# Optimization experiments

Measured on AMD Instinct MI355X. Metric: run time of the kernel, lower is better.

## Reference

```python
import jax, jax.numpy as jnp
import numpy as np

DIM = 2048
NH = 16
NKV = 4
HD = DIM // NH            # 128
KVD = HD * NKV            # 512
MLP = int(DIM * 4.0 * 2 / 3)  # 5461
EPS = 1.1920929e-07       # torch.finfo(float32).eps (nn.RMSNorm default)
ROPE_BASE = 10000.0


def act_quant(x):
    # per-token int8 absmax quantization (BitNet b1.58)
    scale = 127.0 / jnp.clip(jnp.max(jnp.abs(x), axis=-1, keepdims=True), 1e-5)
    return jnp.clip(jnp.round(x * scale), -128.0, 127.0) / scale


def weight_quant(w):
    # ternary weights via mean-absmax scale (BitNet b1.58)
    scale = 1.0 / jnp.clip(jnp.mean(jnp.abs(w)), 1e-5)
    return jnp.clip(jnp.round(w * scale), -1.0, 1.0) / scale


def bitlinear(x, w, b=None):
    # straight-through estimator quantization, then dense matmul
    xq = x + jax.lax.stop_gradient(act_quant(x) - x)
    wq = w + jax.lax.stop_gradient(weight_quant(w) - w)
    y = xq @ wq.T
    return y if b is None else y + b


def rmsnorm(x, w):
    return x * jax.lax.rsqrt(jnp.mean(x * x, axis=-1, keepdims=True) + EPS) * w


def rope_cos_sin(pos, head_dim, dtype):
    inv_freq = 1.0 / (ROPE_BASE ** (jnp.arange(0, head_dim, 2, dtype=jnp.float32) / head_dim))
    freqs = pos[..., None].astype(jnp.float32) * inv_freq  # [B,N,HD/2]
    cos = jnp.repeat(jnp.cos(freqs), 2, axis=-1).astype(dtype)  # interleaved [B,N,HD]
    sin = jnp.repeat(jnp.sin(freqs), 2, axis=-1).astype(dtype)
    return cos, sin


def rotate_interleave(x):
    x1 = x[..., 0::2]
    x2 = x[..., 1::2]
    return jnp.stack([-x2, x1], axis=-1).reshape(x.shape)


def apply_rope(x, cos, sin):
    # x: [B,H,N,HD]; cos/sin: [B,N,HD]
    return x * cos[:, None] + rotate_interleave(x) * sin[:, None]


def setup_inputs() -> dict:
    key = jax.random.key(0)
    ks = jax.random.split(key, 16)
    B, N = 2, 2048
    s = 0.02
    return {
        "x": jax.random.normal(ks[0], (B, N, DIM), jnp.float32),
        "position_ids": jnp.broadcast_to(jnp.arange(N, dtype=jnp.int32), (B, N)),
        "norm1_w": jnp.ones((DIM,), jnp.float32),
        "q_w": jax.random.normal(ks[1], (DIM, DIM), jnp.float32) * s,
        "q_b": jnp.zeros((DIM,), jnp.float32),
        "k_w": jax.random.normal(ks[2], (KVD, DIM), jnp.float32) * s,
        "k_b": jnp.zeros((KVD,), jnp.float32),
        "v_w": jax.random.normal(ks[3], (KVD, DIM), jnp.float32) * s,
        "v_b": jnp.zeros((KVD,), jnp.float32),
        "o_w": jax.random.normal(ks[4], (DIM, DIM), jnp.float32) * s,
        "norm2_w": jnp.ones((DIM,), jnp.float32),
        "gate_w": jax.random.normal(ks[5], (MLP, DIM), jnp.float32) * s,
        "up_w": jax.random.normal(ks[6], (MLP, DIM), jnp.float32) * s,
        "down_w": jax.random.normal(ks[7], (DIM, MLP), jnp.float32) * s,
    }


def reference(x, position_ids, norm1_w, q_w, q_b, k_w, k_b, v_w, v_b, o_w,
              norm2_w, gate_w, up_w, down_w):
    B, N, C = x.shape
    # --- attention ---
    h = rmsnorm(x, norm1_w)
    q = bitlinear(h, q_w, q_b).reshape(B, N, NH, HD).transpose(0, 2, 1, 3)
    k = bitlinear(h, k_w, k_b).reshape(B, N, NKV, HD).transpose(0, 2, 1, 3)
    v = bitlinear(h, v_w, v_b).reshape(B, N, NKV, HD).transpose(0, 2, 1, 3)
    cos, sin = rope_cos_sin(position_ids, HD, x.dtype)
    q = apply_rope(q, cos, sin)
    k = apply_rope(k, cos, sin)
    g = NH // NKV
    k = jnp.repeat(k, g, axis=1)  # GQA head expansion -> [B,NH,N,HD]
    v = jnp.repeat(v, g, axis=1)
    scores = jnp.einsum('bhqd,bhkd->bhqk', q, k) * (HD ** -0.5)
    causal_mask = jnp.triu(jnp.ones((N, N), bool), 1)
    scores = jnp.where(causal_mask, -jnp.inf, scores)
    attn = jax.nn.softmax(scores, axis=-1)
    out = jnp.einsum('bhqk,bhkd->bqhd', attn, v).reshape(B, N, C)
    x = x + bitlinear(out, o_w)
    # --- SwiGLU MLP ---
    h = rmsnorm(x, norm2_w)
    x = x + bitlinear(jax.nn.silu(bitlinear(h, gate_w)) * bitlinear(h, up_w), down_w)
    return x
```

## Files before the change

kernel.cpp:

```cpp
#include <hip/hip_runtime.h>

typedef unsigned short u16;
typedef unsigned int   u32;
typedef unsigned char  u8;

using bf16x8 = __attribute__((ext_vector_type(8))) short;
using f32x4  = __attribute__((ext_vector_type(4))) float;
using i32x4  = __attribute__((ext_vector_type(4))) int;

#define SEQ    2048
#define DIMC   2048
#define TOK    4096
#define QKV_N  3072
#define GU_N   11008
#define MLP_P  5504
#define MLP_R  5461
#define ATT_SCALE 0.08838834764831845f

__device__ __forceinline__ float bf2f(u16 v){ return __uint_as_float(((u32)v) << 16); }
__device__ __forceinline__ u16 f2bf(float f){
  u32 x = __float_as_uint(f);
  u32 r = (x + 0x7fffu + ((x >> 16) & 1u)) >> 16;
  return (u16)r;
}

__device__ __forceinline__ float waveRedSum(float v){
#pragma unroll
  for (int o = 32; o > 0; o >>= 1) v += __shfl_xor(v, o);
  return v;
}
__device__ __forceinline__ float waveRedMax(float v){
#pragma unroll
  for (int o = 32; o > 0; o >>= 1) v = fmaxf(v, __shfl_xor(v, o));
  return v;
}

#define GLD16(gp, lp) __builtin_amdgcn_global_load_lds( \
    (__attribute__((address_space(1))) void*)(gp), \
    (__attribute__((address_space(3))) void*)(lp), 16, 0, 0)

#define FENCE() asm volatile("" ::: "memory")
#define SBAR()  do{ FENCE(); __builtin_amdgcn_s_barrier(); FENCE(); }while(0)
#define VMCNT(n) asm volatile("s_waitcnt vmcnt(" #n ")" ::: "memory")

__global__ __launch_bounds__(256) void k_abssum7(
    const float4* __restrict__ w0, const float4* __restrict__ w1,
    const float4* __restrict__ w2, const float4* __restrict__ w3,
    const float4* __restrict__ w4, const float4* __restrict__ w5,
    const float4* __restrict__ w6, float* __restrict__ sc){
  const int rg = blockIdx.y;
  const float4* w = rg==0?w0: rg==1?w1: rg==2?w2: rg==3?w3: rg==4?w4: rg==5?w5: w6;
  const int n4 = (rg==0||rg==3) ? 1048576 : (rg<4 ? 262144 : 2796032);
  float s = 0.f;
  for (int i = blockIdx.x*256 + threadIdx.x; i < n4; i += gridDim.x*256){
    float4 v = w[i];
    s += fabsf(v.x) + fabsf(v.y) + fabsf(v.z) + fabsf(v.w);
  }
  s = waveRedSum(s);
  __shared__ float sm[4];
  int lane = threadIdx.x & 63, wv = threadIdx.x >> 6;
  if (lane == 0) sm[wv] = s;
  __syncthreads();
  if (threadIdx.x == 0) atomicAdd(sc + rg, sm[0]+sm[1]+sm[2]+sm[3]);
}

__global__ void k_finalize(float* __restrict__ sc){
  if (threadIdx.x == 0){
    const float counts[7] = {4194304.f, 1048576.f, 1048576.f, 4194304.f,
                             11184128.f, 11184128.f, 11184128.f};
    for (int i = 0; i < 7; i++) sc[8+i] = fmaxf(sc[i]/counts[i], 1e-5f);
  }
}

__global__ __launch_bounds__(256) void k_wquant6(
    const float4* __restrict__ w0, const float4* __restrict__ w1,
    const float4* __restrict__ w2, const float4* __restrict__ w3,
    const float4* __restrict__ w4, const float4* __restrict__ w5,
    u32* __restrict__ d0, u32* __restrict__ d1, u32* __restrict__ d2,
    u32* __restrict__ d3, u32* __restrict__ dgu,
    const float* __restrict__ sc){
  const int rg = blockIdx.y;
  const float4* src = rg==0?w0: rg==1?w1: rg==2?w2: rg==3?w3: rg==4?w4: w5;
  const int n4 = (rg==0||rg==3) ? 1048576 : (rg<4 ? 262144 : 2796032);
  float ws = 1.0f / sc[8+rg];
  for (int i = blockIdx.x*256 + threadIdx.x; i < n4; i += gridDim.x*256){
    float4 v = src[i];
    int c0 = (int)fminf(fmaxf(rintf(v.x*ws), -1.f), 1.f);
    int c1 = (int)fminf(fmaxf(rintf(v.y*ws), -1.f), 1.f);
    int c2 = (int)fminf(fmaxf(rintf(v.z*ws), -1.f), 1.f);
    int c3 = (int)fminf(fmaxf(rintf(v.w*ws), -1.f), 1.f);
    u32 pk = (u32)(u8)c0 | ((u32)(u8)c1 << 8) | ((u32)(u8)c2 << 16) | ((u32)(u8)c3 << 24);
    if (rg < 4){
      u32* dst = rg==0?d0: rg==1?d1: rg==2?d2: d3;
      dst[i] = pk;
    } else {
      int row = i >> 9, col = i & 511;
      int rI = 32*(row>>4) + (row&15) + ((rg==5)?16:0);
      dgu[(long)rI*512 + col] = pk;
    }
  }
}

__global__ __launch_bounds__(256) void k_wquant_down(const float* __restrict__ src,
                                                     u32* __restrict__ dst,
                                                     const float* __restrict__ deqp){
  int i = blockIdx.x*256 + threadIdx.x;
  const int total = 2048*(MLP_P/4);
  if (i >= total) return;
  float ws = 1.0f / deqp[0];
  int r = i / (MLP_P/4);
  int c4 = (i - r*(MLP_P/4))*4;
  u32 o = 0;
#pragma unroll
  for (int e = 0; e < 4; e++){
    int c = c4 + e;
    int t = 0;
    if (c < MLP_R) t = (int)fminf(fmaxf(rintf(src[(long)r*MLP_R + c]*ws), -1.f), 1.f);
    o |= (u32)(u8)t << (8*e);
  }
  dst[i] = o;
}

__global__ __launch_bounds__(256) void k_rmsq(const float* __restrict__ in,
                                              const float* __restrict__ nw,
                                              char* __restrict__ outq,
                                              float* __restrict__ rowdeq, int do_norm){
  const int row = blockIdx.x, tid = threadIdx.x;
  const float* xp = in + (long)row * DIMC + tid*8;
  float v[8];
  float4 a0 = *(const float4*)xp;
  float4 a1 = *(const float4*)(xp + 4);
  v[0]=a0.x; v[1]=a0.y; v[2]=a0.z; v[3]=a0.w;
  v[4]=a1.x; v[5]=a1.y; v[6]=a1.z; v[7]=a1.w;
  float ss = 0.f;
#pragma unroll
  for (int j = 0; j < 8; j++) ss += v[j]*v[j];
  __shared__ float sm[8];
  int lane = tid & 63, wv = tid >> 6;
  ss = waveRedSum(ss);
  if (lane == 0) sm[wv] = ss;
  __syncthreads();
  float h[8];
  float amax = 0.f;
  if (do_norm){
    float tot = sm[0]+sm[1]+sm[2]+sm[3];
    float rms = rsqrtf(tot * (1.0f/DIMC) + 1.1920929e-07f);
    float4 w0 = *(const float4*)(nw + tid*8);
    float4 w1 = *(const float4*)(nw + tid*8 + 4);
    float wr8[8] = {w0.x,w0.y,w0.z,w0.w,w1.x,w1.y,w1.z,w1.w};
#pragma unroll
    for (int j = 0; j < 8; j++){ h[j] = v[j]*rms*wr8[j]; amax = fmaxf(amax, fabsf(h[j])); }
  } else {
#pragma unroll
    for (int j = 0; j < 8; j++){ h[j] = v[j]; amax = fmaxf(amax, fabsf(h[j])); }
  }
  amax = waveRedMax(amax);
  if (lane == 0) sm[4+wv] = amax;
  __syncthreads();
  float gmax = fmaxf(fmaxf(sm[4],sm[5]), fmaxf(sm[6],sm[7]));
  float sc = 127.0f / fmaxf(gmax, 1e-5f);
  int2 o;
  char* oc = (char*)&o;
#pragma unroll
  for (int j = 0; j < 8; j++)
    oc[j] = (char)(int)fminf(fmaxf(rintf(h[j]*sc), -128.f), 127.f);
  *(int2*)(outq + (long)row*DIMC + tid*8) = o;
  if (tid == 0) rowdeq[row] = 1.0f / sc;
}

__global__ __launch_bounds__(256) void k_ropevt2(u16* __restrict__ y,
                                                 const int* __restrict__ pos_ids,
                                                 u16* __restrict__ VT){
  if (blockIdx.x < 4096){
    const int m = blockIdx.x, tid = threadIdx.x;
    __shared__ float cs[64], sn[64];
    if (tid < 64){
      float pos = (float)pos_ids[m];
      float inv = expf((float)tid * -0.14391156831212787f);
      float s, c;
      sincosf(pos * inv, &s, &c);
      cs[tid] = c; sn[tid] = s;
    }
    __syncthreads();
    u32* row = (u32*)(y + (long)m*QKV_N);
#pragma unroll
    for (int it = 0; it < 5; it++){
      int p = it*256 + tid;
      int i = p & 63;
      u32 both = row[p];
      float x0 = bf2f((u16)(both & 0xffffu));
      float x1 = bf2f((u16)(both >> 16));
      float c = cs[i], s = sn[i];
      u16 o0 = f2bf(x0*c - x1*s);
      u16 o1 = f2bf(x1*c + x0*s);
      row[p] = (u32)o0 | ((u32)o1 << 16);
    }
  } else {
    int idx = (int)(blockIdx.x - 4096)*256 + threadIdx.x;
    int d  = idx & 127;
    int hk = (idx >> 7) & 3;
    int b  = (idx >> 9) & 1;
    int tg = idx >> 10;
    int tok0 = tg*8;
    const u16* src = y + ((long)b*SEQ + tok0)*QKV_N + 2560 + hk*128 + d;
    u16 tmp[8];
#pragma unroll
    for (int e = 0; e < 8; e++) tmp[e] = src[(long)e*QKV_N];
    *(int4*)(VT + (((long)(b*4+hk))*128 + d)*SEQ + tok0) = *(int4*)tmp;
  }
}

template<int BM, int BN, int WM, int WN, int MODE>
__global__ __launch_bounds__(512, 2) void k_gemm8(
    const char* __restrict__ A, const char* __restrict__ B,
    int K, int lda, int ldb, int ldc, int ntn,
    const float* __restrict__ rowdeq, const float* __restrict__ deqp,
    const float* __restrict__ bq, const float* __restrict__ bk, const float* __restrict__ bv,
    const float* __restrict__ resid, float* __restrict__ outF, u16* __restrict__ outB)
{
  constexpr int SM = BM/WM, SN = BN/WN;
  constexpr int MR = SM/16, NR = SN/16, MRH = MR/2;
  constexpr int RA = BM/128, RB = BN/128;
  constexpr int ASZ = BM*64, BSZ = BN*64;
  constexpr int BUFSZ = 2*(ASZ+BSZ);
  extern __shared__ __align__(16) char sm8[];

  const int tid = threadIdx.x;
  const int lane = tid & 63, wv = tid >> 6;
  const int wr = wv / WN, wc = wv % WN;
  const int r = lane & 15, qq = lane >> 4;

  const int nwg = gridDim.x;
  const int chunk = nwg >> 3;
  const int lin = blockIdx.x;
  const int swz = (lin & 7)*chunk + (lin >> 3);
  const int mt = swz / ntn, nt = swz - mt*ntn;
  const long m0 = (long)mt*BM, n0 = (long)nt*BN;

  const char* __restrict__ gA = A + m0*lda;
  const char* __restrict__ gB = B + n0*ldb;

  int  soA[RA], soB[RB];
  long goA[RA], goB[RB];
#pragma unroll
  for (int u = 0; u < RA; u++){
    int c = u*512 + tid, row = c >> 2, gp = c & 3, g = gp ^ ((row>>1)&3);
    soA[u] = c*16; goA[u] = (long)row*lda + g*16;
  }
#pragma unroll
  for (int u = 0; u < RB; u++){
    int c = u*512 + tid, row = c >> 2, gp = c & 3, g = gp ^ ((row>>1)&3);
    soB[u] = c*16; goB[u] = (long)row*ldb + g*16;
  }
  const int gsw = (qq ^ ((r>>1)&3))*16;
  const int aoff0 = (wr*SM + r)*64 + gsw;
  const int boff0 = (wc*SN + r)*64 + gsw;

  const int NT = K >> 7;

  i32x4 acc[MR][NR];
#pragma unroll
  for (int i = 0; i < MR; i++)
#pragma unroll
    for (int j = 0; j < NR; j++) acc[i][j] = (i32x4){0,0,0,0};

  auto stA = [&](int tq, int kh){
    char* dst = sm8 + (tq&1)*BUFSZ + kh*ASZ;
    const char* src = gA + (long)tq*128 + kh*64;
#pragma unroll
    for (int u = 0; u < RA; u++) GLD16(src + goA[u], dst + soA[u]);
  };
  auto stB = [&](int tq, int kh){
    char* dst = sm8 + (tq&1)*BUFSZ + 2*ASZ + kh*BSZ;
    const char* src = gB + (long)tq*128 + kh*64;
#pragma unroll
    for (int u = 0; u < RB; u++) GLD16(src + goB[u], dst + soB[u]);
  };

  stA(0,0); stB(0,0); stA(0,1); stB(0,1);
  stA(1,0); stB(1,0);
  if constexpr (RA+RB == 4) VMCNT(4); else VMCNT(3);
  SBAR();

  for (int t = 0; t < NT; t++){
    const char* cA = sm8 + (t&1)*BUFSZ;
    const char* cB = cA + 2*ASZ;
    i32x4 bF[NR];
    {
      i32x4 aF[MRH];
#pragma unroll
      for (int i = 0; i < MRH; i++) aF[i] = *(const i32x4*)(cA + aoff0 + i*1024);
#pragma unroll
      for (int j = 0; j < NR; j++)  bF[j] = *(const i32x4*)(cB + boff0 + j*1024);
      if (t+1 < NT) stA(t+1, 1);
      SBAR();
      __builtin_amdgcn_s_setprio(1);
#pragma unroll
      for (int i = 0; i < MRH; i++)
#pragma unroll
        for (int j = 0; j < NR; j++)
          acc[i][j] = __builtin_amdgcn_mfma_i32_16x16x64_i8(aF[i], bF[j], acc[i][j], 0,0,0);
      __builtin_amdgcn_s_setprio(0);
      SBAR();
    }
    {
      i32x4 aF[MRH];
#pragma unroll
      for (int i = 0; i < MRH; i++) aF[i] = *(const i32x4*)(cA + aoff0 + (MRH+i)*1024);
      if (t+1 < NT) stB(t+1, 1);
      SBAR();
      __builtin_amdgcn_s_setprio(1);
#pragma unroll
      for (int i = 0; i < MRH; i++)
#pragma unroll
        for (int j = 0; j < NR; j++)
          acc[MRH+i][j] = __builtin_amdgcn_mfma_i32_16x16x64_i8(aF[i], bF[j], acc[MRH+i][j], 0,0,0);
      __builtin_amdgcn_s_setprio(0);
      SBAR();
    }
    {
      i32x4 aF[MRH];
#pragma unroll
      for (int i = 0; i < MRH; i++) aF[i] = *(const i32x4*)(cA + ASZ + aoff0 + i*1024);
#pragma unroll
      for (int j = 0; j < NR; j++)  bF[j] = *(const i32x4*)(cB + BSZ + boff0 + j*1024);
      if (t+2 < NT) stA(t+2, 0);
      SBAR();
      __builtin_amdgcn_s_setprio(1);
#pragma unroll
      for (int i = 0; i < MRH; i++)
#pragma unroll
        for (int j = 0; j < NR; j++)
          acc[i][j] = __builtin_amdgcn_mfma_i32_16x16x64_i8(aF[i], bF[j], acc[i][j], 0,0,0);
      __builtin_amdgcn_s_setprio(0);
      SBAR();
    }
    {
      i32x4 aF[MRH];
#pragma unroll
      for (int i = 0; i < MRH; i++) aF[i] = *(const i32x4*)(cA + ASZ + aoff0 + (MRH+i)*1024);
      if (t+2 < NT) stB(t+2, 0);
      SBAR();
      __builtin_amdgcn_s_setprio(1);
#pragma unroll
      for (int i = 0; i < MRH; i++)
#pragma unroll
        for (int j = 0; j < NR; j++)
          acc[MRH+i][j] = __builtin_amdgcn_mfma_i32_16x16x64_i8(aF[i], bF[j], acc[MRH+i][j], 0,0,0);
      __builtin_amdgcn_s_setprio(0);
      if (t + 1 < NT){
        if (t + 2 < NT){ if constexpr (RA+RB == 4) VMCNT(4); else VMCNT(3); }
        else VMCNT(0);
      }
      SBAR();
    }
  }

#pragma unroll
  for (int i = 0; i < MR; i++){
#pragma unroll
    for (int tt = 0; tt < 4; tt++){
      const long row = m0 + wr*SM + 16*i + 4*qq + tt;
      const float rdv = rowdeq[row];
#pragma unroll
      for (int j = 0; j < NR; j++){
        const long col = n0 + wc*SN + 16*j + r;
        float vv = (float)acc[i][j][tt];
        if constexpr (MODE == 0){
          int sec = (col >= 2048) + (col >= 2560);
          float dq = deqp[sec];
          float bias = (sec == 0) ? bq[col] : (sec == 1) ? bk[col-2048] : bv[col-2560];
          outB[row*(long)ldc + col] = f2bf(vv*rdv*dq + bias);
        } else {
          outF[row*(long)ldc + col] = vv*rdv*deqp[0] + resid[row*(long)ldc + col];
        }
      }
    }
  }
}

template<int MODE>
__global__ __launch_bounds__(256, 2) void k_gemm2b(
    const char* __restrict__ A, const char* __restrict__ B,
    int K, int lda, int ldb, int ldc, int ntn,
    const float* __restrict__ rowdeq, const float* __restrict__ deqp,
    u16* __restrict__ outB)
{
  constexpr int BM = 256, BN = 128;
  constexpr int MR = 8, NR = 4, MRH = 4;
  constexpr int RA = 4, RB = 2;
  constexpr int ASZ = BM*64, BSZ = BN*64;
  constexpr int BUFSZ = ASZ + BSZ;
  __shared__ __align__(16) char sm8[2*BUFSZ];

  const int tid = threadIdx.x;
  const int lane = tid & 63, wv = tid >> 6;
  const int wr = wv >> 1, wc = wv & 1;
  const int r = lane & 15, qq = lane >> 4;

  const int nwg = gridDim.x;
  const int chunk = nwg >> 3;
  const int lin = blockIdx.x;
  const int swz = (lin & 7)*chunk + (lin >> 3);
  const int mt = swz / ntn, nt = swz - mt*ntn;
  const long m0 = (long)mt*BM, n0 = (long)nt*BN;

  const char* __restrict__ gA = A + m0*lda;
  const char* __restrict__ gB = B + n0*ldb;

  int  soA[RA], soB[RB];
  long goA[RA], goB[RB];
#pragma unroll
  for (int u = 0; u < RA; u++){
    int c = u*256 + tid, row = c >> 2, g = (c & 3) ^ ((row>>1)&3);
    soA[u] = c*16; goA[u] = (long)row*lda + g*16;
  }
#pragma unroll
  for (int u = 0; u < RB; u++){
    int c = u*256 + tid, row = c >> 2, g = (c & 3) ^ ((row>>1)&3);
    soB[u] = c*16; goB[u] = (long)row*ldb + g*16;
  }
  const int gsw = (qq ^ ((r>>1)&3))*16;
  const int aoff0 = (wr*128 + r)*64 + gsw;
  const int boff0 = (wc*64 + r)*64 + gsw;

  const int NT = K >> 6;

  i32x4 acc[MR][NR];
#pragma unroll
  for (int i = 0; i < MR; i++)
#pragma unroll
    for (int j = 0; j < NR; j++) acc[i][j] = (i32x4){0,0,0,0};

  auto stA = [&](int tq){
    char* dst = sm8 + (tq&1)*BUFSZ;
    const char* src = gA + (long)tq*64;
#pragma unroll
    for (int u = 0; u < RA; u++) GLD16(src + goA[u], dst + soA[u]);
  };
  auto stB = [&](int tq){
    char* dst = sm8 + (tq&1)*BUFSZ + ASZ;
    const char* src = gB + (long)tq*64;
#pragma unroll
    for (int u = 0; u < RB; u++) GLD16(src + goB[u], dst + soB[u]);
  };

  stA(0); stB(0); stB(1);
  VMCNT(2);
  SBAR();

  for (int t = 0; t < NT; t++){
    const char* cA = sm8 + (t&1)*BUFSZ;
    const char* cB = cA + ASZ;
    i32x4 bF[NR];
    {
      i32x4 aF[MRH];
#pragma unroll
      for (int i = 0; i < MRH; i++) aF[i] = *(const i32x4*)(cA + aoff0 + i*1024);
#pragma unroll
      for (int j = 0; j < NR; j++)  bF[j] = *(const i32x4*)(cB + boff0 + j*1024);
      if (t+1 < NT) stA(t+1);
      SBAR();
      __builtin_amdgcn_s_setprio(1);
#pragma unroll
      for (int i = 0; i < MRH; i++)
#pragma unroll
        for (int j = 0; j < NR; j++)
          acc[i][j] = __builtin_amdgcn_mfma_i32_16x16x64_i8(aF[i], bF[j], acc[i][j], 0,0,0);
      __builtin_amdgcn_s_setprio(0);
      SBAR();
    }
    {
      i32x4 aF[MRH];
#pragma unroll
      for (int i = 0; i < MRH; i++) aF[i] = *(const i32x4*)(cA + aoff0 + (MRH+i)*1024);
      if (t+2 < NT) stB(t+2);
      SBAR();
      __builtin_amdgcn_s_setprio(1);
#pragma unroll
      for (int i = 0; i < MRH; i++)
#pragma unroll
        for (int j = 0; j < NR; j++)
          acc[MRH+i][j] = __builtin_amdgcn_mfma_i32_16x16x64_i8(aF[i], bF[j], acc[MRH+i][j], 0,0,0);
      __builtin_amdgcn_s_setprio(0);
      if (t + 1 < NT){
        if (t + 2 < NT) VMCNT(2); else VMCNT(0);
      }
      SBAR();
    }
  }

  const float dqg = deqp[0], dqu = deqp[1];
#pragma unroll
  for (int i = 0; i < MR; i++){
#pragma unroll
    for (int tt = 0; tt < 4; tt++){
      const long row = m0 + wr*128 + 16*i + 4*qq + tt;
      const float rdv = rowdeq[row];
#pragma unroll
      for (int j = 0; j < NR; j += 2){
        const long col = n0 + wc*64 + 16*j + r;
        float g = (float)acc[i][j][tt]   * rdv * dqg;
        float u = (float)acc[i][j+1][tt] * rdv * dqu;
        float hv = g * (1.0f/(1.0f + __expf(-g))) * u;
        const long hcol = (col >> 5)*16 + (col & 15);
        outB[row*(long)ldc + hcol] = f2bf(hv);
      }
    }
  }
}

__global__ __launch_bounds__(256) void k_attn(const u16* __restrict__ Y,
                                              const u16* __restrict__ VT,
                                              float* __restrict__ O)
{
  __shared__ u16 Ks[64*128];
  __shared__ u16 VTs[128*64];
  __shared__ u16 Ps[64][72];

  const int pp = blockIdx.x;
  const int bh = blockIdx.y;
  const int b = bh >> 4, h = bh & 15, hk = h >> 2;
  const int tid = threadIdx.x;
  const int lane = tid & 63, wv = tid >> 6;
  const int r = lane & 15, qq = lane >> 4;
  const long rowbase = (long)b * SEQ;
  const u16* Kbase = Y + rowbase*QKV_N + 2048 + hk*128;
  const u16* Vbase = VT + ((long)(b*4+hk))*128*SEQ;

  for (int ph = 0; ph < 2; ph++){
    const int qt = ph ? pp : 31 - pp;
    const int q0 = qt * 64;

    bf16x8 qf[4];
#pragma unroll
    for (int kc = 0; kc < 4; kc++)
      qf[kc] = *(const bf16x8*)(Y + (rowbase + q0 + wv*16 + r)*QKV_N + h*128 + kc*32 + qq*8);

#pragma unroll
    for (int rnd = 0; rnd < 4; rnd++){
      int c = rnd*256 + tid;
      int row = c >> 4, g = (c & 15) ^ (row & 7);
      GLD16(Kbase + ((long)(qt*0 + row))*QKV_N + g*8, (char*)Ks + c*16);
    }
#pragma unroll
    for (int rnd = 0; rnd < 4; rnd++){
      int c = rnd*256 + tid;
      int d = c >> 3, g = (c & 7) ^ (d & 7);
      GLD16(Vbase + (long)d*SEQ + g*8, (char*)VTs + c*16);
    }
    __syncthreads();

    f32x4 accO[8];
#pragma unroll
    for (int jn = 0; jn < 8; jn++) accO[jn] = (f32x4){0.f,0.f,0.f,0.f};
    float m_run[4] = {-INFINITY,-INFINITY,-INFINITY,-INFINITY};
    float l_run[4] = {0.f,0.f,0.f,0.f};

    for (int kt = 0; kt <= qt; kt++){
      float sv[4][4];
#pragma unroll
      for (int j = 0; j < 4; j++){
        f32x4 a = (f32x4){0.f,0.f,0.f,0.f};
#pragma unroll
        for (int kc = 0; kc < 4; kc++){
          bf16x8 kf = *(const bf16x8*)(Ks + (16*j + r)*128 + (((kc*4 + qq) ^ (r & 7)))*8);
          a = __builtin_amdgcn_mfma_f32_16x16x32_bf16(qf[kc], kf, a, 0, 0, 0);
        }
#pragma unroll
        for (int t = 0; t < 4; t++) sv[j][t] = a[t] * ATT_SCALE;
      }
      __syncthreads();
      if (kt < qt){
#pragma unroll
        for (int rnd = 0; rnd < 4; rnd++){
          int c = rnd*256 + tid;
          int row = c >> 4, g = (c & 15) ^ (row & 7);
          GLD16(Kbase + ((long)((kt+1)*64 + row))*QKV_N + g*8, (char*)Ks + c*16);
        }
      }
      if (kt == qt){
#pragma unroll
        for (int j = 0; j < 4; j++){
          int key = kt*64 + 16*j + r;
#pragma unroll
          for (int t = 0; t < 4; t++){
            int qr = q0 + wv*16 + 4*qq + t;
            if (key > qr) sv[j][t] = -INFINITY;
          }
        }
      }
#pragma unroll
      for (int t = 0; t < 4; t++){
        float mm = fmaxf(fmaxf(sv[0][t],sv[1][t]), fmaxf(sv[2][t],sv[3][t]));
#pragma unroll
        for (int o = 8; o > 0; o >>= 1) mm = fmaxf(mm, __shfl_xor(mm, o));
        float mnew = fmaxf(m_run[t], mm);
        float alpha = __expf(m_run[t] - mnew);
        m_run[t] = mnew;
        float ps = 0.f;
#pragma unroll
        for (int j = 0; j < 4; j++){
          float p = __expf(sv[j][t] - mnew);
          ps += p;
          Ps[wv*16 + 4*qq + t][16*j + r] = f2bf(p);
        }
#pragma unroll
        for (int o = 8; o > 0; o >>= 1) ps += __shfl_xor(ps, o);
        l_run[t] = l_run[t]*alpha + ps;
#pragma unroll
        for (int jn = 0; jn < 8; jn++) accO[jn][t] *= alpha;
      }
#pragma unroll
      for (int kc = 0; kc < 2; kc++){
        bf16x8 pf = *(const bf16x8*)&Ps[wv*16 + r][kc*32 + qq*8];
#pragma unroll
        for (int jn = 0; jn < 8; jn++){
          bf16x8 vf = *(const bf16x8*)(VTs + (16*jn + r)*64 + (((kc*4 + qq) ^ (r & 7)))*8);
          accO[jn] = __builtin_amdgcn_mfma_f32_16x16x32_bf16(pf, vf, accO[jn], 0, 0, 0);
        }
      }
      __syncthreads();
      if (kt < qt){
#pragma unroll
        for (int rnd = 0; rnd < 4; rnd++){
          int c = rnd*256 + tid;
          int d = c >> 3, g = (c & 7) ^ (d & 7);
          GLD16(Vbase + (long)d*SEQ + (kt+1)*64 + g*8, (char*)VTs + c*16);
        }
      }
    }
    float inv[4];
#pragma unroll
    for (int t = 0; t < 4; t++) inv[t] = 1.0f / l_run[t];
#pragma unroll
    for (int jn = 0; jn < 8; jn++){
#pragma unroll
      for (int t = 0; t < 4; t++){
        long row = rowbase + q0 + wv*16 + 4*qq + t;
        O[row*DIMC + h*128 + 16*jn + r] = accO[jn][t]*inv[t];
      }
    }
    __syncthreads();
  }
}

__global__ __launch_bounds__(256) void k_hquant(const u16* __restrict__ hbuf,
                                                char* __restrict__ qout,
                                                float* __restrict__ rowdeq){
  const int row = blockIdx.x, tid = threadIdx.x;
  const u16* base = hbuf + (long)row * MLP_P;
  float h[24];
  float amax = 0.f;
#pragma unroll
  for (int it = 0; it < 3; it++){
    int chunk = it*256 + tid;
    if (chunk < 688){
      int j0 = chunk*8;
      int4 h4 = *(const int4*)(base + j0);
      const u16* hp = (const u16*)&h4;
#pragma unroll
      for (int e = 0; e < 8; e++){
        float hv = bf2f(hp[e]);
        h[it*8+e] = hv;
        amax = fmaxf(amax, fabsf(hv));
      }
    } else {
#pragma unroll
      for (int e = 0; e < 8; e++) h[it*8+e] = 0.f;
    }
  }
  amax = waveRedMax(amax);
  __shared__ float sm[4];
  int lane = tid & 63, wv = tid >> 6;
  if (lane == 0) sm[wv] = amax;
  __syncthreads();
  float gmax = fmaxf(fmaxf(sm[0],sm[1]), fmaxf(sm[2],sm[3]));
  float sc = 127.0f / fmaxf(gmax, 1e-5f);
#pragma unroll
  for (int it = 0; it < 3; it++){
    int chunk = it*256 + tid;
    if (chunk < 688){
      int j0 = chunk*8;
      int2 o;
      char* oc = (char*)&o;
#pragma unroll
      for (int e = 0; e < 8; e++)
        oc[e] = (char)(int)fminf(fmaxf(rintf(h[it*8+e]*sc), -128.f), 127.f);
      *(int2*)(qout + (long)row*MLP_P + j0) = o;
    }
  }
  if (tid == 0) rowdeq[row] = 1.0f/sc;
}

extern "C" void kernel_launch(void* const* d_in, const int* in_sizes, int n_in,
                              void* d_out, int out_size, void* d_ws, size_t ws_size,
                              hipStream_t stream)
{
  (void)in_sizes; (void)n_in; (void)out_size; (void)ws_size;
  const float* x   = (const float*)d_in[0];
  const int*   pos = (const int*)d_in[1];
  const float* n1w = (const float*)d_in[2];
  const float* qw  = (const float*)d_in[3];
  const float* qb  = (const float*)d_in[4];
  const float* kw  = (const float*)d_in[5];
  const float* kb  = (const float*)d_in[6];
  const float* vw  = (const float*)d_in[7];
  const float* vb  = (const float*)d_in[8];
  const float* ow  = (const float*)d_in[9];
  const float* n2w = (const float*)d_in[10];
  const float* gw  = (const float*)d_in[11];
  const float* uw  = (const float*)d_in[12];
  const float* dw  = (const float*)d_in[13];
  float* out = (float*)d_out;
  char* ws = (char*)d_ws;

  static int attr_done = 0;
  if (!attr_done){
    hipFuncSetAttribute(reinterpret_cast<const void*>(k_gemm8<256,128,4,2,0>),
                        hipFuncAttributeMaxDynamicSharedMemorySize, 98304);
    hipFuncSetAttribute(reinterpret_cast<const void*>(k_gemm8<256,128,4,2,1>),
                        hipFuncAttributeMaxDynamicSharedMemorySize, 98304);
    attr_done = 1;
  }

  float* sc   = (float*)ws;
  char* Wqkv  = ws + 256;
  char* Wo    = ws + 6291712;
  char* Wgu   = ws + 10486016;
  char* Wd    = ws + 33030400;
  char* actq  = ws + 44302592;
  char* swq   = ws + 52691200;
  float* rd   = (float*)(ws + 75235584);
  char* xreg  = ws + 75252224;
  u16* yqkv   = (u16*)xreg;
  float* attn = (float*)(xreg + 25165824);
  u16* vT     = (u16*)(xreg + 58720256);
  u16* hbuf   = (u16*)xreg;

  hipMemsetAsync(sc, 0, 64, stream);
  hipMemsetAsync(Wgu, 0, 11008l*2048, stream);
  k_abssum7<<<dim3(512,7),256,0,stream>>>((const float4*)qw, (const float4*)kw,
                                          (const float4*)vw, (const float4*)ow,
                                          (const float4*)gw, (const float4*)uw,
                                          (const float4*)dw, sc);
  k_finalize<<<1,64,0,stream>>>(sc);
  k_wquant6<<<dim3(512,6),256,0,stream>>>((const float4*)qw, (const float4*)kw,
                                          (const float4*)vw, (const float4*)ow,
                                          (const float4*)gw, (const float4*)uw,
                                          (u32*)Wqkv, (u32*)(Wqkv + 2048l*2048),
                                          (u32*)(Wqkv + 2560l*2048), (u32*)Wo,
                                          (u32*)Wgu, sc);
  k_wquant_down<<<11008,256,0,stream>>>(dw, (u32*)Wd, sc+14);

  k_rmsq<<<4096,256,0,stream>>>(x, n1w, actq, rd, 1);
  k_gemm8<256,128,4,2,0><<<384,512,98304,stream>>>(actq, Wqkv, 2048, 2048, 2048, 3072, 24,
                                          rd, sc+8, qb, kb, vb, nullptr, nullptr, yqkv);
  k_ropevt2<<<5120,256,0,stream>>>(yqkv, pos, vT);
  k_attn<<<dim3(16,32),256,0,stream>>>(yqkv, vT, attn);
  k_rmsq<<<4096,256,0,stream>>>(attn, n1w, actq, rd, 0);
  k_gemm8<256,128,4,2,1><<<256,512,98304,stream>>>(actq, Wo, 2048, 2048, 2048, 2048, 16,
                                          rd, sc+11, nullptr, nullptr, nullptr, x, out, nullptr);

  k_rmsq<<<4096,256,0,stream>>>(out, n2w, actq, rd, 1);
  k_gemm2b<3><<<1376,256,0,stream>>>(actq, Wgu, 2048, 2048, 2048, MLP_P, 86,
                                     rd, sc+12, hbuf);
  k_hquant<<<4096,256,0,stream>>>(hbuf, swq, rd);
  k_gemm8<256,128,4,2,1><<<256,512,98304,stream>>>(swq, Wd, 5504, 5504, 5504, 2048, 16,
                                          rd, sc+14, nullptr, nullptr, nullptr, out, out, nullptr);
}
```

Measured before the change: 670.2 us.

## Use bf16 attention output, smaller-tile gemm for O/down, XCD-aware gate/up tiling

The attention kernel now writes bf16 output, and a simpler quantization kernel reads it, dropping the norm-free fp32 path and halving that traffic. The O-projection and down-projection GEMMs switch from the 512-thread 256x128 gemm8 to a templated k_gemm2b with BM=128, which launches more workgroups at a higher occupancy target. The gate/up GEMM gets an XCD-aware tile mapping so each XCD covers a contiguous range of N tiles, padded to 88 with early exit. Risks include bf16 rounding of the attention output before quantization and different tile efficiency.

```diff
diff --git a/kernel.cpp b/kernel.cpp
--- a/kernel.cpp
+++ b/kernel.cpp
@@ -168,6 +168,32 @@
   if (tid == 0) rowdeq[row] = 1.0f / sc;
 }
 
+__global__ __launch_bounds__(256) void k_quantb(const u16* __restrict__ in,
+                                                char* __restrict__ outq,
+                                                float* __restrict__ rowdeq){
+  const int row = blockIdx.x, tid = threadIdx.x;
+  int4 a = *(const int4*)(in + (long)row*DIMC + tid*8);
+  const u16* ap = (const u16*)&a;
+  float v[8];
+  float amax = 0.f;
+#pragma unroll
+  for (int j = 0; j < 8; j++){ v[j] = bf2f(ap[j]); amax = fmaxf(amax, fabsf(v[j])); }
+  amax = waveRedMax(amax);
+  __shared__ float sm[4];
+  int lane = tid & 63, wv = tid >> 6;
+  if (lane == 0) sm[wv] = amax;
+  __syncthreads();
+  float gmax = fmaxf(fmaxf(sm[0],sm[1]), fmaxf(sm[2],sm[3]));
+  float sc = 127.0f / fmaxf(gmax, 1e-5f);
+  int2 o;
+  char* oc = (char*)&o;
+#pragma unroll
+  for (int j = 0; j < 8; j++)
+    oc[j] = (char)(int)fminf(fmaxf(rintf(v[j]*sc), -128.f), 127.f);
+  *(int2*)(outq + (long)row*DIMC + tid*8) = o;
+  if (tid == 0) rowdeq[row] = 1.0f / sc;
+}
+
 __global__ __launch_bounds__(256) void k_ropevt2(u16* __restrict__ y,
                                                  const int* __restrict__ pos_ids,
                                                  u16* __restrict__ VT){
@@ -379,16 +405,17 @@
   }
 }
 
-template<int MODE>
-__global__ __launch_bounds__(256, 2) void k_gemm2b(
+template<int BM, int MODE>
+__global__ __launch_bounds__(256, (BM==128)?3:2) void k_gemm2b(
     const char* __restrict__ A, const char* __restrict__ B,
-    int K, int lda, int ldb, int ldc, int ntn,
+    int K, int lda, int ldb, int ldc, int vnt, int ntreal,
     const float* __restrict__ rowdeq, const float* __restrict__ deqp,
+    const float* __restrict__ resid, float* __restrict__ outF,
     u16* __restrict__ outB)
 {
-  constexpr int BM = 256, BN = 128;
-  constexpr int MR = 8, NR = 4, MRH = 4;
-  constexpr int RA = 4, RB = 2;
+  constexpr int BN = 128;
+  constexpr int MR = BM/32, NR = 4, MRH = MR/2;
+  constexpr int RA = BM/64, RB = 2;
   constexpr int ASZ = BM*64, BSZ = BN*64;
   constexpr int BUFSZ = ASZ + BSZ;
   __shared__ __align__(16) char sm8[2*BUFSZ];
@@ -398,11 +425,19 @@
   const int wr = wv >> 1, wc = wv & 1;
   const int r = lane & 15, qq = lane >> 4;
 
-  const int nwg = gridDim.x;
-  const int chunk = nwg >> 3;
+  int mt, nt;
   const int lin = blockIdx.x;
-  const int swz = (lin & 7)*chunk + (lin >> 3);
-  const int mt = swz / ntn, nt = swz - mt*ntn;
+  if constexpr (MODE == 3){
+    const int xcd = lin & 7, i0 = lin >> 3;
+    const int xcdw = vnt >> 3;
+    const int ntl = i0 % xcdw; mt = i0 / xcdw;
+    nt = xcd*xcdw + ntl;
+    if (nt >= ntreal) return;
+  } else {
+    const int chunk = gridDim.x >> 3;
+    const int swz = (lin & 7)*chunk + (lin >> 3);
+    mt = swz / vnt; nt = swz - mt*vnt;
+  }
   const long m0 = (long)mt*BM, n0 = (long)nt*BN;
 
   const char* __restrict__ gA = A + m0*lda;
@@ -421,7 +456,7 @@
     soB[u] = c*16; goB[u] = (long)row*ldb + g*16;
   }
   const int gsw = (qq ^ ((r>>1)&3))*16;
-  const int aoff0 = (wr*128 + r)*64 + gsw;
+  const int aoff0 = (wr*(BM/2) + r)*64 + gsw;
   const int boff0 = (wc*64 + r)*64 + gsw;
 
   const int NT = K >> 6;
@@ -490,21 +525,30 @@
     }
   }
 
-  const float dqg = deqp[0], dqu = deqp[1];
 #pragma unroll
   for (int i = 0; i < MR; i++){
 #pragma unroll
     for (int tt = 0; tt < 4; tt++){
-      const long row = m0 + wr*128 + 16*i + 4*qq + tt;
+      const long row = m0 + wr*(BM/2) + 16*i + 4*qq + tt;
       const float rdv = rowdeq[row];
-#pragma unroll
-      for (int j = 0; j < NR; j += 2){
-        const long col = n0 + wc*64 + 16*j + r;
-        float g = (float)acc[i][j][tt]   * rdv * dqg;
-        float u = (float)acc[i][j+1][tt] * rdv * dqu;
-        float hv = g * (1.0f/(1.0f + __expf(-g))) * u;
-        const long hcol = (col >> 5)*16 + (col & 15);
-        outB[row*(long)ldc + hcol] = f2bf(hv);
+      if constexpr (MODE == 3){
+        const float dqg = deqp[0], dqu = deqp[1];
+#pragma unroll
+        for (int j = 0; j < NR; j += 2){
+          const long col = n0 + wc*64 + 16*j + r;
+          float g = (float)acc[i][j][tt]   * rdv * dqg;
+          float u = (float)acc[i][j+1][tt] * rdv * dqu;
+          float hv = g * (1.0f/(1.0f + __expf(-g))) * u;
+          const long hcol = (col >> 5)*16 + (col & 15);
+          outB[row*(long)ldc + hcol] = f2bf(hv);
+        }
+      } else {
+#pragma unroll
+        for (int j = 0; j < NR; j++){
+          const long col = n0 + wc*64 + 16*j + r;
+          float vv = (float)acc[i][j][tt];
+          outF[row*(long)ldc + col] = vv*rdv*deqp[0] + resid[row*(long)ldc + col];
+        }
       }
     }
   }
@@ -512,7 +556,7 @@
 
 __global__ __launch_bounds__(256) void k_attn(const u16* __restrict__ Y,
                                               const u16* __restrict__ VT,
-                                              float* __restrict__ O)
+                                              u16* __restrict__ O)
 {
   __shared__ u16 Ks[64*128];
   __shared__ u16 VTs[128*64];
@@ -638,7 +682,7 @@
 #pragma unroll
       for (int t = 0; t < 4; t++){
         long row = rowbase + q0 + wv*16 + 4*qq + t;
-        O[row*DIMC + h*128 + 16*jn + r] = accO[jn][t]*inv[t];
+        O[row*DIMC + h*128 + 16*jn + r] = f2bf(accO[jn][t]*inv[t]);
       }
     }
     __syncthreads();
@@ -719,8 +763,6 @@
   if (!attr_done){
     hipFuncSetAttribute(reinterpret_cast<const void*>(k_gemm8<256,128,4,2,0>),
                         hipFuncAttributeMaxDynamicSharedMemorySize, 98304);
-    hipFuncSetAttribute(reinterpret_cast<const void*>(k_gemm8<256,128,4,2,1>),
-                        hipFuncAttributeMaxDynamicSharedMemorySize, 98304);
     attr_done = 1;
   }
 
@@ -734,7 +776,7 @@
   float* rd   = (float*)(ws + 75235584);
   char* xreg  = ws + 75252224;
   u16* yqkv   = (u16*)xreg;
-  float* attn = (float*)(xreg + 25165824);
+  u16* attnb  = (u16*)(xreg + 25165824);
   u16* vT     = (u16*)(xreg + 58720256);
   u16* hbuf   = (u16*)xreg;
 
@@ -757,15 +799,15 @@
   k_gemm8<256,128,4,2,0><<<384,512,98304,stream>>>(actq, Wqkv, 2048, 2048, 2048, 3072, 24,
                                           rd, sc+8, qb, kb, vb, nullptr, nullptr, yqkv);
   k_ropevt2<<<5120,256,0,stream>>>(yqkv, pos, vT);
-  k_attn<<<dim3(16,32),256,0,stream>>>(yqkv, vT, attn);
-  k_rmsq<<<4096,256,0,stream>>>(attn, n1w, actq, rd, 0);
-  k_gemm8<256,128,4,2,1><<<256,512,98304,stream>>>(actq, Wo, 2048, 2048, 2048, 2048, 16,
-                                          rd, sc+11, nullptr, nullptr, nullptr, x, out, nullptr);
+  k_attn<<<dim3(16,32),256,0,stream>>>(yqkv, vT, attnb);
+  k_quantb<<<4096,256,0,stream>>>(attnb, actq, rd);
+  k_gemm2b<128,1><<<512,256,0,stream>>>(actq, Wo, 2048, 2048, 2048, 2048, 16, 16,
+                                        rd, sc+11, x, out, nullptr);
 
   k_rmsq<<<4096,256,0,stream>>>(out, n2w, actq, rd, 1);
-  k_gemm2b<3><<<1376,256,0,stream>>>(actq, Wgu, 2048, 2048, 2048, MLP_P, 86,
-                                     rd, sc+12, hbuf);
+  k_gemm2b<256,3><<<1408,256,0,stream>>>(actq, Wgu, 2048, 2048, 2048, MLP_P, 88, 86,
+                                         rd, sc+12, nullptr, nullptr, hbuf);
   k_hquant<<<4096,256,0,stream>>>(hbuf, swq, rd);
-  k_gemm8<256,128,4,2,1><<<256,512,98304,stream>>>(swq, Wd, 5504, 5504, 5504, 2048, 16,
-                                          rd, sc+14, nullptr, nullptr, nullptr, out, out, nullptr);
-}
+  k_gemm2b<128,1><<<512,256,0,stream>>>(swq, Wd, 5504, 5504, 5504, 2048, 16, 16,
+                                        rd, sc+14, out, out, nullptr);
+}
```

Measured after the change: 673.5 us. No clear change (+0.5%).
